# Kernel tuning notes

Hardware: AMD Instinct MI355X
Metric: run time of the kernel (lower is better)

Reference implementation:

```python
import jax, jax.numpy as jnp
import numpy as np

NET_W = 416.0
NET_H = 416.0
OBJ_THRESH = 0.5
COORD_SCALE = 5.0
NOOBJ_SCALE = 1.0
OBJ_SCALE = 5.0
CLASS_SCALE = 1.0


def setup_inputs() -> dict:
    key = jax.random.key(0)
    k1, k2, k3, k4, k5, k6, k7 = jax.random.split(key, 7)
    B, A, C, gh, gw = 32, 5, 80, 52, 52
    HW = gh * gw
    net_out = jax.random.normal(k1, (B, gh, gw, A * (5 + C)), dtype=jnp.float32)
    anchors = jnp.array([[10., 13.], [33., 23.], [62., 45.], [116., 90.], [373., 326.]], dtype=jnp.float32)
    obj_cell = (jax.random.uniform(k2, (B, HW)) < 0.01).astype(jnp.float32)  # [B,HW]
    a_idx = jax.random.randint(k3, (B, HW), 0, A)
    a_onehot = jax.nn.one_hot(a_idx, A, axis=1, dtype=jnp.float32)  # [B,A,HW]
    anchor_mask = (obj_cell[:, None, :] * a_onehot)[:, :, None, :]  # [B,A,1,HW]
    obj_mask = (obj_cell[:, None, :] * jnp.ones((1, A, 1), jnp.float32))  # [B,A,HW]
    # targets: [x_off, y_off, w_log, h_log, conf, class] per anchor/cell, zero where unassigned
    t_xy = jax.random.uniform(k4, (B, A, 2, HW), dtype=jnp.float32)
    t_wh = 0.5 * jax.random.normal(k5, (B, A, 2, HW), dtype=jnp.float32)
    t_conf = jax.random.uniform(k6, (B, A, 1, HW), dtype=jnp.float32)
    t_cls = jax.random.randint(k7, (B, A, 1, HW), 0, C).astype(jnp.float32)
    targets = jnp.concatenate([t_xy, t_wh, t_conf, t_cls], axis=2) * anchor_mask
    return {"net_out": net_out, "targets": targets, "anchor_mask": anchor_mask,
            "obj_mask": obj_mask, "anchors": anchors}


def _to_grid(coords, col, row, gw, gh, aw, ah):
    # coords: [B,A,4,HW] (xy offsets in-cell, wh in log space) -> corner boxes [B,A,4,HW]
    cx = (coords[:, :, 0, :] + col) / gw * NET_W
    cy = (coords[:, :, 1, :] + row) / gh * NET_H
    w = jnp.exp(coords[:, :, 2, :]) * aw
    h = jnp.exp(coords[:, :, 3, :]) * ah
    x1 = cx - 0.5 * w
    y1 = cy - 0.5 * h
    return jnp.stack([x1, y1, x1 + w, y1 + h], axis=2)


def _yolo_loss(net_out, targets, anchor_mask, obj_mask, anchors):
    B, gh, gw, oc = net_out.shape
    A = anchors.shape[0]
    C = oc // A - 5
    HW = gh * gw
    p = net_out.reshape(B, A, 5 + C, HW)
    xy = jax.nn.sigmoid(p[:, :, :2, :])            # [B,A,2,HW]
    wh = p[:, :, 2:4, :]                           # raw log-space
    conf = jax.nn.sigmoid(p[:, :, 4, :])           # [B,A,HW]
    logits = p[:, :, 5:, :]                        # [B,A,C,HW]
    conf_mask = anchor_mask[:, :, 0, :]            # [B,A,HW]

    # class cross-entropy, masked to responsible anchors
    logp = jax.nn.log_softmax(logits, axis=2)
    t_cls = targets[:, :, 5, :].astype(jnp.int32)  # [B,A,HW]
    ce = -jnp.take_along_axis(logp, t_cls[:, :, None, :], axis=2)[:, :, 0, :]
    clas_loss = (ce * conf_mask).sum()

    aw = anchors[:, 0][None, :, None]
    ah = anchors[:, 1][None, :, None]
    true_xy = targets[:, :, 0:2, :]
    true_wh = targets[:, :, 2:4, :]
    t_wscale = jnp.exp(true_wh[:, :, 0, :]) * aw / NET_W
    t_hscale = jnp.exp(true_wh[:, :, 1, :]) * ah / NET_H
    p_wscale = jnp.exp(wh[:, :, 0, :]) * aw / NET_W
    p_hscale = jnp.exp(wh[:, :, 1, :]) * ah / NET_H
    xy_loss = (jnp.square(xy - true_xy) * anchor_mask).sum()
    wh_loss = (jnp.square(p_wscale - t_wscale) * conf_mask).sum() \
            + (jnp.square(p_hscale - t_hscale) * conf_mask).sum()
    coords_loss = xy_loss + wh_loss

    t_conf = targets[:, :, 4, :]
    diff2 = jnp.square(conf - t_conf)
    obj_conf_loss = (diff2 * conf_mask).sum()
    noobj1 = diff2 * (1.0 - obj_mask)
    no_resp = (1.0 - conf_mask) * obj_mask

    hw = jnp.arange(HW)
    col = (hw % gw).astype(jnp.float32)
    row = (hw // gw).astype(jnp.float32)
    pred_boxes = _to_grid(jnp.concatenate([xy, wh], axis=2), col, row, gw, gh, aw, ah)
    gt_boxes = _to_grid(targets[:, :, :4, :], col, row, gw, gh, aw, ah)
    iw = jnp.maximum(jnp.minimum(pred_boxes[:, :, 2, :], gt_boxes[:, :, 2, :])
                     - jnp.maximum(pred_boxes[:, :, 0, :], gt_boxes[:, :, 0, :]), 0.0)
    ih = jnp.maximum(jnp.minimum(pred_boxes[:, :, 3, :], gt_boxes[:, :, 3, :])
                     - jnp.maximum(pred_boxes[:, :, 1, :], gt_boxes[:, :, 1, :]), 0.0)
    inter = iw * ih
    area_p = (pred_boxes[:, :, 2, :] - pred_boxes[:, :, 0, :]) * (pred_boxes[:, :, 3, :] - pred_boxes[:, :, 1, :])
    area_g = (gt_boxes[:, :, 2, :] - gt_boxes[:, :, 0, :]) * (gt_boxes[:, :, 3, :] - gt_boxes[:, :, 1, :])
    iou = inter / (area_p + area_g - inter + 1e-9)
    iou_lt = (iou < OBJ_THRESH).astype(jnp.float32)
    noobj_conf_loss = (noobj1 + diff2 * no_resp * iou_lt).sum()

    total = (clas_loss * CLASS_SCALE + coords_loss * COORD_SCALE
             + obj_conf_loss * OBJ_SCALE + noobj_conf_loss * NOOBJ_SCALE)
    return total


def reference(net_out, targets, anchor_mask, obj_mask, anchors):
    return _yolo_loss(net_out, targets, anchor_mask, obj_mask, anchors)
```

## Files before the change

### kernel.cpp

```cpp
#include <hip/hip_runtime.h>


constexpr int B_  = 32;
constexpr int A_  = 5;
constexpr int C_  = 80;
constexpr int GW_ = 52;
constexpr int GH_ = 52;
constexpr int HW_ = GW_ * GH_;
constexpr int NCH = 5 + C_;
constexpr int TOTAL = B_ * A_ * HW_;
constexpr int BLOCK = 256;
constexpr int GRID  = TOTAL / BLOCK;

constexpr float NET_W = 416.0f;
constexpr float NET_H = 416.0f;
constexpr float OBJ_THRESH  = 0.5f;
constexpr float COORD_SCALE = 5.0f;
constexpr float NOOBJ_SCALE = 1.0f;
constexpr float OBJ_SCALE   = 5.0f;
constexpr float CLASS_SCALE = 1.0f;

__device__ __forceinline__ float sigmoidf_(float x) {
    return 1.0f / (1.0f + __expf(-x));
}

__global__ __launch_bounds__(256) void yolo_partial_kernel(
    const float* __restrict__ net,
    const float* __restrict__ tgt,
    const float* __restrict__ amask,
    const float* __restrict__ omask,
    const float* __restrict__ anchors,
    float* __restrict__ partial)
{
    const int i    = blockIdx.x * blockDim.x + threadIdx.x;
    const int lane = threadIdx.x & 63;

    const int hw = i % HW_;
    const int ba = i / HW_;
    const int a  = ba % A_;

    const unsigned nbase = (unsigned)ba * (unsigned)(NCH * HW_) + (unsigned)hw;
    const unsigned tbase = (unsigned)ba * (unsigned)(6 * HW_)   + (unsigned)hw;

    const float cm = amask[i];
    const float om = omask[i];

    const bool want_ce  = (cm != 0.0f);
    const bool need_box = want_ce || (om != 0.0f);

    const float conf = sigmoidf_(net[nbase + 4u * HW_]);
    float t_conf = 0.0f;
    if (want_ce) t_conf = tgt[tbase + 4u * HW_];
    const float d     = conf - t_conf;
    const float diff2 = d * d;

    float loss = diff2 * (1.0f - om) * NOOBJ_SCALE;

    int tc = 0;
    if (need_box) {
        const float aw = anchors[2 * a];
        const float ah = anchors[2 * a + 1];

        const float p0 = net[nbase + 0u * HW_];
        const float p1 = net[nbase + 1u * HW_];
        const float p2 = net[nbase + 2u * HW_];
        const float p3 = net[nbase + 3u * HW_];
        const float t0 = tgt[tbase + 0u * HW_];
        const float t1 = tgt[tbase + 1u * HW_];
        const float t2 = tgt[tbase + 2u * HW_];
        const float t3 = tgt[tbase + 3u * HW_];

        const float sx = sigmoidf_(p0);
        const float sy = sigmoidf_(p1);

        if (want_ce) {
            const float dx = sx - t0;
            const float dy = sy - t1;
            const float pws = __expf(p2) * aw * (1.0f / NET_W);
            const float phs = __expf(p3) * ah * (1.0f / NET_H);
            const float tws = __expf(t2) * aw * (1.0f / NET_W);
            const float ths = __expf(t3) * ah * (1.0f / NET_H);
            const float dw = pws - tws;
            const float dh = phs - ths;
            loss += (dx * dx + dy * dy + dw * dw + dh * dh) * COORD_SCALE;
            loss += diff2 * OBJ_SCALE;
            tc = (int)tgt[tbase + 5u * HW_];
        } else {
            const float col = (float)(hw % GW_);
            const float row = (float)(hw / GW_);

            const float pcx = (sx + col) * (NET_W / (float)GW_);
            const float pcy = (sy + row) * (NET_H / (float)GH_);
            const float pw  = __expf(p2) * aw;
            const float ph  = __expf(p3) * ah;
            const float px1 = pcx - 0.5f * pw;
            const float py1 = pcy - 0.5f * ph;
            const float px2 = px1 + pw;
            const float py2 = py1 + ph;

            const float gcx = (t0 + col) * (NET_W / (float)GW_);
            const float gcy = (t1 + row) * (NET_H / (float)GH_);
            const float gwd = __expf(t2) * aw;
            const float ghd = __expf(t3) * ah;
            const float gx1 = gcx - 0.5f * gwd;
            const float gy1 = gcy - 0.5f * ghd;
            const float gx2 = gx1 + gwd;
            const float gy2 = gy1 + ghd;

            const float iw = fmaxf(fminf(px2, gx2) - fmaxf(px1, gx1), 0.0f);
            const float ih = fmaxf(fminf(py2, gy2) - fmaxf(py1, gy1), 0.0f);
            const float inter  = iw * ih;
            const float area_p = (px2 - px1) * (py2 - py1);
            const float area_g = (gx2 - gx1) * (gy2 - gy1);
            const float iou = inter / (area_p + area_g - inter + 1e-9f);
            if (iou < OBJ_THRESH) {
                loss += diff2 * NOOBJ_SCALE;
            }
        }
    }

    unsigned long long m = __ballot(want_ce);
    while (m) {
        const int src = __ffsll((long long)m) - 1;
        m &= m - 1;
        const unsigned nb  = (unsigned)__shfl((int)nbase, src, 64);
        const int      tcs = __shfl(tc, src, 64);

        const float x0 = net[nb + (unsigned)(5 + lane) * HW_];
        const float x1 = (lane < 16) ? net[nb + (unsigned)(69 + lane) * HW_]
                                     : -1e30f;

        float mx = fmaxf(x0, x1);
        #pragma unroll
        for (int off = 32; off > 0; off >>= 1)
            mx = fmaxf(mx, __shfl_xor(mx, off, 64));

        float s = __expf(x0 - mx) + ((lane < 16) ? __expf(x1 - mx) : 0.0f);
        #pragma unroll
        for (int off = 32; off > 0; off >>= 1)
            s += __shfl_xor(s, off, 64);

        const int  idx = (tcs < 64) ? tcs : (tcs - 64);
        const float xa = __shfl(x0, idx, 64);
        const float xb = __shfl(x1, idx, 64);
        const float xt = (tcs < 64) ? xa : xb;

        const float ce = -(xt - mx - __logf(s));
        if (lane == src) loss += ce * CLASS_SCALE;
    }

    #pragma unroll
    for (int off = 32; off > 0; off >>= 1)
        loss += __shfl_down(loss, off, 64);

    __shared__ float wsum[4];
    const int wid = threadIdx.x >> 6;
    if (lane == 0) wsum[wid] = loss;
    __syncthreads();
    if (threadIdx.x == 0)
        partial[blockIdx.x] = wsum[0] + wsum[1] + wsum[2] + wsum[3];
}

__global__ __launch_bounds__(256) void yolo_reduce_kernel(
    const float* __restrict__ partial, float* __restrict__ out)
{
    float s = 0.0f;
    for (int j = threadIdx.x; j < GRID; j += BLOCK)
        s += partial[j];

    #pragma unroll
    for (int off = 32; off > 0; off >>= 1)
        s += __shfl_down(s, off, 64);

    __shared__ float w[4];
    const int lane = threadIdx.x & 63;
    const int wid  = threadIdx.x >> 6;
    if (lane == 0) w[wid] = s;
    __syncthreads();
    if (threadIdx.x == 0)
        out[0] = w[0] + w[1] + w[2] + w[3];
}

extern "C" void kernel_launch(void* const* d_in, const int* in_sizes, int n_in,
                              void* d_out, int out_size, void* d_ws, size_t ws_size,
                              hipStream_t stream) {
    const float* net     = (const float*)d_in[0];
    const float* tgt     = (const float*)d_in[1];
    const float* amask   = (const float*)d_in[2];
    const float* omask   = (const float*)d_in[3];
    const float* anchors = (const float*)d_in[4];
    float* out     = (float*)d_out;
    float* partial = (float*)d_ws;

    yolo_partial_kernel<<<GRID, BLOCK, 0, stream>>>(net, tgt, amask, omask, anchors, partial);
    yolo_reduce_kernel<<<1, BLOCK, 0, stream>>>(partial, out);
}
```

Before: 11.94 us.

## Process two cells per thread, pair softmax rows, fuse reduction via atomics

```diff
diff --git a/kernel.cpp b/kernel.cpp
--- a/kernel.cpp
+++ b/kernel.cpp
@@ -10,7 +10,8 @@
 constexpr int NCH = 5 + C_;
 constexpr int TOTAL = B_ * A_ * HW_;
 constexpr int BLOCK = 256;
-constexpr int GRID  = TOTAL / BLOCK;
+constexpr int CPT   = 2;
+constexpr int GRID  = TOTAL / (BLOCK * CPT);
 
 constexpr float NET_W = 416.0f;
 constexpr float NET_H = 416.0f;
@@ -24,129 +25,185 @@
     return 1.0f / (1.0f + __expf(-x));
 }
 
-__global__ __launch_bounds__(256) void yolo_partial_kernel(
+__device__ __forceinline__ float cell_terms(
+    const float* __restrict__ net, const float* __restrict__ tgt,
+    unsigned nbase, unsigned tbase, int hw, float aw, float ah,
+    float cm, float om, float diff2, bool want_ce, int& tc)
+{
+    float loss = diff2 * (1.0f - om) * NOOBJ_SCALE;
+
+    const bool need_box = want_ce || (om != 0.0f);
+    if (!need_box) return loss;
+
+    const float p0 = net[nbase + 0u * HW_];
+    const float p1 = net[nbase + 1u * HW_];
+    const float p2 = net[nbase + 2u * HW_];
+    const float p3 = net[nbase + 3u * HW_];
+    const float t0 = tgt[tbase + 0u * HW_];
+    const float t1 = tgt[tbase + 1u * HW_];
+    const float t2 = tgt[tbase + 2u * HW_];
+    const float t3 = tgt[tbase + 3u * HW_];
+
+    const float sx = sigmoidf_(p0);
+    const float sy = sigmoidf_(p1);
+
+    if (want_ce) {
+        const float dx = sx - t0;
+        const float dy = sy - t1;
+        const float pws = __expf(p2) * aw * (1.0f / NET_W);
+        const float phs = __expf(p3) * ah * (1.0f / NET_H);
+        const float tws = __expf(t2) * aw * (1.0f / NET_W);
+        const float ths = __expf(t3) * ah * (1.0f / NET_H);
+        const float dw = pws - tws;
+        const float dh = phs - ths;
+        loss += (dx * dx + dy * dy + dw * dw + dh * dh) * COORD_SCALE;
+        loss += diff2 * OBJ_SCALE;
+        tc = (int)tgt[tbase + 5u * HW_];
+    } else {
+        const float col = (float)(hw % GW_);
+        const float row = (float)(hw / GW_);
+
+        const float pcx = (sx + col) * (NET_W / (float)GW_);
+        const float pcy = (sy + row) * (NET_H / (float)GH_);
+        const float pw  = __expf(p2) * aw;
+        const float ph  = __expf(p3) * ah;
+        const float px1 = pcx - 0.5f * pw;
+        const float py1 = pcy - 0.5f * ph;
+        const float px2 = px1 + pw;
+        const float py2 = py1 + ph;
+
+        const float gcx = (t0 + col) * (NET_W / (float)GW_);
+        const float gcy = (t1 + row) * (NET_H / (float)GH_);
+        const float gwd = __expf(t2) * aw;
+        const float ghd = __expf(t3) * ah;
+        const float gx1 = gcx - 0.5f * gwd;
+        const float gy1 = gcy - 0.5f * ghd;
+        const float gx2 = gx1 + gwd;
+        const float gy2 = gy1 + ghd;
+
+        const float iw = fmaxf(fminf(px2, gx2) - fmaxf(px1, gx1), 0.0f);
+        const float ih = fmaxf(fminf(py2, gy2) - fmaxf(py1, gy1), 0.0f);
+        const float inter  = iw * ih;
+        const float area_p = (px2 - px1) * (py2 - py1);
+        const float area_g = (gx2 - gx1) * (gy2 - gy1);
+        const float iou = inter / (area_p + area_g - inter + 1e-9f);
+        if (iou < OBJ_THRESH) loss += diff2 * NOOBJ_SCALE;
+    }
+    return loss;
+}
+
+__global__ __launch_bounds__(256) void yolo_loss_kernel(
     const float* __restrict__ net,
     const float* __restrict__ tgt,
     const float* __restrict__ amask,
     const float* __restrict__ omask,
     const float* __restrict__ anchors,
-    float* __restrict__ partial)
+    float* __restrict__ out)
 {
-    const int i    = blockIdx.x * blockDim.x + threadIdx.x;
+    const int t    = blockIdx.x * blockDim.x + threadIdx.x;
     const int lane = threadIdx.x & 63;
 
-    const int hw = i % HW_;
-    const int ba = i / HW_;
-    const int a  = ba % A_;
-
-    const unsigned nbase = (unsigned)ba * (unsigned)(NCH * HW_) + (unsigned)hw;
-    const unsigned tbase = (unsigned)ba * (unsigned)(6 * HW_)   + (unsigned)hw;
-
-    const float cm = amask[i];
-    const float om = omask[i];
-
-    const bool want_ce  = (cm != 0.0f);
-    const bool need_box = want_ce || (om != 0.0f);
-
-    const float conf = sigmoidf_(net[nbase + 4u * HW_]);
-    float t_conf = 0.0f;
-    if (want_ce) t_conf = tgt[tbase + 4u * HW_];
-    const float d     = conf - t_conf;
-    const float diff2 = d * d;
-
-    float loss = diff2 * (1.0f - om) * NOOBJ_SCALE;
-
-    int tc = 0;
-    if (need_box) {
-        const float aw = anchors[2 * a];
-        const float ah = anchors[2 * a + 1];
-
-        const float p0 = net[nbase + 0u * HW_];
-        const float p1 = net[nbase + 1u * HW_];
-        const float p2 = net[nbase + 2u * HW_];
-        const float p3 = net[nbase + 3u * HW_];
-        const float t0 = tgt[tbase + 0u * HW_];
-        const float t1 = tgt[tbase + 1u * HW_];
-        const float t2 = tgt[tbase + 2u * HW_];
-        const float t3 = tgt[tbase + 3u * HW_];
-
-        const float sx = sigmoidf_(p0);
-        const float sy = sigmoidf_(p1);
-
-        if (want_ce) {
-            const float dx = sx - t0;
-            const float dy = sy - t1;
-            const float pws = __expf(p2) * aw * (1.0f / NET_W);
-            const float phs = __expf(p3) * ah * (1.0f / NET_H);
-            const float tws = __expf(t2) * aw * (1.0f / NET_W);
-            const float ths = __expf(t3) * ah * (1.0f / NET_H);
-            const float dw = pws - tws;
-            const float dh = phs - ths;
-            loss += (dx * dx + dy * dy + dw * dw + dh * dh) * COORD_SCALE;
-            loss += diff2 * OBJ_SCALE;
-            tc = (int)tgt[tbase + 5u * HW_];
-        } else {
-            const float col = (float)(hw % GW_);
-            const float row = (float)(hw / GW_);
-
-            const float pcx = (sx + col) * (NET_W / (float)GW_);
-            const float pcy = (sy + row) * (NET_H / (float)GH_);
-            const float pw  = __expf(p2) * aw;
-            const float ph  = __expf(p3) * ah;
-            const float px1 = pcx - 0.5f * pw;
-            const float py1 = pcy - 0.5f * ph;
-            const float px2 = px1 + pw;
-            const float py2 = py1 + ph;
-
-            const float gcx = (t0 + col) * (NET_W / (float)GW_);
-            const float gcy = (t1 + row) * (NET_H / (float)GH_);
-            const float gwd = __expf(t2) * aw;
-            const float ghd = __expf(t3) * ah;
-            const float gx1 = gcx - 0.5f * gwd;
-            const float gy1 = gcy - 0.5f * ghd;
-            const float gx2 = gx1 + gwd;
-            const float gy2 = gy1 + ghd;
-
-            const float iw = fmaxf(fminf(px2, gx2) - fmaxf(px1, gx1), 0.0f);
-            const float ih = fmaxf(fminf(py2, gy2) - fmaxf(py1, gy1), 0.0f);
-            const float inter  = iw * ih;
-            const float area_p = (px2 - px1) * (py2 - py1);
-            const float area_g = (gx2 - gx1) * (gy2 - gy1);
-            const float iou = inter / (area_p + area_g - inter + 1e-9f);
-            if (iou < OBJ_THRESH) {
-                loss += diff2 * NOOBJ_SCALE;
+    const int cell0 = 2 * t;
+    const int hw0   = cell0 % HW_;
+    const int ba    = cell0 / HW_;
+    const int a     = ba % A_;
+
+    const unsigned nbase0 = (unsigned)ba * (unsigned)(NCH * HW_) + (unsigned)hw0;
+    const unsigned tbase0 = (unsigned)ba * (unsigned)(6 * HW_)   + (unsigned)hw0;
+
+    const float2 am2 = *reinterpret_cast<const float2*>(amask + cell0);
+    const float2 om2 = *reinterpret_cast<const float2*>(omask + cell0);
+    const float2 cf2 = *reinterpret_cast<const float2*>(net + nbase0 + 4u * HW_);
+
+    const float aw = anchors[2 * a];
+    const float ah = anchors[2 * a + 1];
+
+    float loss = 0.0f;
+    int   tc0 = 0, tc1 = 0;
+
+    const bool ce0 = (am2.x != 0.0f);
+    {
+        const float conf  = sigmoidf_(cf2.x);
+        const float tcf   = ce0 ? tgt[tbase0 + 4u * HW_] : 0.0f;
+        const float d     = conf - tcf;
+        const float diff2 = d * d;
+        loss += cell_terms(net, tgt, nbase0, tbase0, hw0, aw, ah,
+                           am2.x, om2.x, diff2, ce0, tc0);
+        if (ce0) loss += 0.0f;
+    }
+    const bool ce1 = (am2.y != 0.0f);
+    {
+        const float conf  = sigmoidf_(cf2.y);
+        const float tcf   = ce1 ? tgt[tbase0 + 1u + 4u * HW_] : 0.0f;
+        const float d     = conf - tcf;
+        const float diff2 = d * d;
+        loss += cell_terms(net, tgt, nbase0 + 1u, tbase0 + 1u, hw0 + 1, aw, ah,
+                           am2.y, om2.y, diff2, ce1, tc1);
+    }
+
+    {
+        unsigned long long m0 = __ballot(ce0);
+        unsigned long long m1 = __ballot(ce1);
+        const int nb0i = (int)nbase0;
+        while (m0 | m1) {
+            int srcA, slotA;
+            if (m0) { srcA = __ffsll((long long)m0) - 1; slotA = 0; m0 &= m0 - 1; }
+            else    { srcA = __ffsll((long long)m1) - 1; slotA = 1; m1 &= m1 - 1; }
+            const bool hasB = (m0 | m1) != 0ull;
+            int srcB = 0, slotB = 0;
+            if (hasB) {
+                if (m0) { srcB = __ffsll((long long)m0) - 1; slotB = 0; m0 &= m0 - 1; }
+                else    { srcB = __ffsll((long long)m1) - 1; slotB = 1; m1 &= m1 - 1; }
+            }
+
+            const unsigned nbA = (unsigned)__shfl(nb0i, srcA, 64) + (unsigned)slotA;
+            const int      tcA = slotA ? __shfl(tc1, srcA, 64) : __shfl(tc0, srcA, 64);
+
+            const float xA0 = net[nbA + (unsigned)(5 + lane) * HW_];
+            const float xA1 = (lane < 16) ? net[nbA + (unsigned)(69 + lane) * HW_] : -1e30f;
+
+            float xB0 = 0.0f, xB1 = -1e30f;
+            unsigned nbB = 0; int tcB = 0;
+            if (hasB) {
+                nbB = (unsigned)__shfl(nb0i, srcB, 64) + (unsigned)slotB;
+                tcB = slotB ? __shfl(tc1, srcB, 64) : __shfl(tc0, srcB, 64);
+                xB0 = net[nbB + (unsigned)(5 + lane) * HW_];
+                xB1 = (lane < 16) ? net[nbB + (unsigned)(69 + lane) * HW_] : -1e30f;
+            }
+
+            {
+                float mx = fmaxf(xA0, xA1);
+                #pragma unroll
+                for (int off = 32; off > 0; off >>= 1)
+                    mx = fmaxf(mx, __shfl_xor(mx, off, 64));
+                float s = __expf(xA0 - mx) + ((lane < 16) ? __expf(xA1 - mx) : 0.0f);
+                #pragma unroll
+                for (int off = 32; off > 0; off >>= 1)
+                    s += __shfl_xor(s, off, 64);
+                const int idx = (tcA < 64) ? tcA : (tcA - 64);
+                const float xa = __shfl(xA0, idx, 64);
+                const float xb = __shfl(xA1, idx, 64);
+                const float xt = (tcA < 64) ? xa : xb;
+                const float ce = -(xt - mx - __logf(s));
+                if (lane == srcA) loss += ce * CLASS_SCALE;
+            }
+            if (hasB) {
+                float mx = fmaxf(xB0, xB1);
+                #pragma unroll
+                for (int off = 32; off > 0; off >>= 1)
+                    mx = fmaxf(mx, __shfl_xor(mx, off, 64));
+                float s = __expf(xB0 - mx) + ((lane < 16) ? __expf(xB1 - mx) : 0.0f);
+                #pragma unroll
+                for (int off = 32; off > 0; off >>= 1)
+                    s += __shfl_xor(s, off, 64);
+                const int idx = (tcB < 64) ? tcB : (tcB - 64);
+                const float xa = __shfl(xB0, idx, 64);
+                const float xb = __shfl(xB1, idx, 64);
+                const float xt = (tcB < 64) ? xa : xb;
+                const float ce = -(xt - mx - __logf(s));
+                if (lane == srcB) loss += ce * CLASS_SCALE;
             }
         }
-    }
-
-    unsigned long long m = __ballot(want_ce);
-    while (m) {
-        const int src = __ffsll((long long)m) - 1;
-        m &= m - 1;
-        const unsigned nb  = (unsigned)__shfl((int)nbase, src, 64);
-        const int      tcs = __shfl(tc, src, 64);
-
-        const float x0 = net[nb + (unsigned)(5 + lane) * HW_];
-        const float x1 = (lane < 16) ? net[nb + (unsigned)(69 + lane) * HW_]
-                                     : -1e30f;
-
-        float mx = fmaxf(x0, x1);
-        #pragma unroll
-        for (int off = 32; off > 0; off >>= 1)
-            mx = fmaxf(mx, __shfl_xor(mx, off, 64));
-
-        float s = __expf(x0 - mx) + ((lane < 16) ? __expf(x1 - mx) : 0.0f);
-        #pragma unroll
-        for (int off = 32; off > 0; off >>= 1)
-            s += __shfl_xor(s, off, 64);
-
-        const int  idx = (tcs < 64) ? tcs : (tcs - 64);
-        const float xa = __shfl(x0, idx, 64);
-        const float xb = __shfl(x1, idx, 64);
-        const float xt = (tcs < 64) ? xa : xb;
-
-        const float ce = -(xt - mx - __logf(s));
-        if (lane == src) loss += ce * CLASS_SCALE;
     }
 
     #pragma unroll
@@ -158,27 +215,7 @@
     if (lane == 0) wsum[wid] = loss;
     __syncthreads();
     if (threadIdx.x == 0)
-        partial[blockIdx.x] = wsum[0] + wsum[1] + wsum[2] + wsum[3];
-}
-
-__global__ __launch_bounds__(256) void yolo_reduce_kernel(
-    const float* __restrict__ partial, float* __restrict__ out)
-{
-    float s = 0.0f;
-    for (int j = threadIdx.x; j < GRID; j += BLOCK)
-        s += partial[j];
-
-    #pragma unroll
-    for (int off = 32; off > 0; off >>= 1)
-        s += __shfl_down(s, off, 64);
-
-    __shared__ float w[4];
-    const int lane = threadIdx.x & 63;
-    const int wid  = threadIdx.x >> 6;
-    if (lane == 0) w[wid] = s;
-    __syncthreads();
-    if (threadIdx.x == 0)
-        out[0] = w[0] + w[1] + w[2] + w[3];
+        atomicAdd(out, wsum[0] + wsum[1] + wsum[2] + wsum[3]);
 }
 
 extern "C" void kernel_launch(void* const* d_in, const int* in_sizes, int n_in,
@@ -189,9 +226,9 @@
     const float* amask   = (const float*)d_in[2];
     const float* omask   = (const float*)d_in[3];
     const float* anchors = (const float*)d_in[4];
-    float* out     = (float*)d_out;
-    float* partial = (float*)d_ws;
-
-    yolo_partial_kernel<<<GRID, BLOCK, 0, stream>>>(net, tgt, amask, omask, anchors, partial);
-    yolo_reduce_kernel<<<1, BLOCK, 0, stream>>>(partial, out);
-}
+    float* out = (float*)d_out;
+
+    hipMemsetAsync(out, 0, sizeof(float), stream);
+
+    yolo_loss_kernel<<<GRID, BLOCK, 0, stream>>>(net, tgt, amask, omask, anchors, out);
+}
```

After: 23.18 us. 1.94x slower.

## Fuse final reduction via last-block counter and batch four CE rows per wave

Applied to the files above, without the earlier changes.

```diff
diff --git a/kernel.cpp b/kernel.cpp
--- a/kernel.cpp
+++ b/kernel.cpp
@@ -24,13 +24,15 @@
     return 1.0f / (1.0f + __expf(-x));
 }
 
-__global__ __launch_bounds__(256) void yolo_partial_kernel(
+__global__ __launch_bounds__(256) void yolo_loss_kernel(
     const float* __restrict__ net,
     const float* __restrict__ tgt,
     const float* __restrict__ amask,
     const float* __restrict__ omask,
     const float* __restrict__ anchors,
-    float* __restrict__ partial)
+    float* __restrict__ partial,
+    unsigned* __restrict__ counter,
+    float* __restrict__ out)
 {
     const int i    = blockIdx.x * blockDim.x + threadIdx.x;
     const int lane = threadIdx.x & 63;
@@ -113,40 +115,63 @@
             const float area_p = (px2 - px1) * (py2 - py1);
             const float area_g = (gx2 - gx1) * (gy2 - gy1);
             const float iou = inter / (area_p + area_g - inter + 1e-9f);
-            if (iou < OBJ_THRESH) {
-                loss += diff2 * NOOBJ_SCALE;
-            }
+            if (iou < OBJ_THRESH) loss += diff2 * NOOBJ_SCALE;
         }
     }
 
-    unsigned long long m = __ballot(want_ce);
-    while (m) {
-        const int src = __ffsll((long long)m) - 1;
-        m &= m - 1;
-        const unsigned nb  = (unsigned)__shfl((int)nbase, src, 64);
-        const int      tcs = __shfl(tc, src, 64);
-
-        const float x0 = net[nb + (unsigned)(5 + lane) * HW_];
-        const float x1 = (lane < 16) ? net[nb + (unsigned)(69 + lane) * HW_]
-                                     : -1e30f;
-
-        float mx = fmaxf(x0, x1);
-        #pragma unroll
-        for (int off = 32; off > 0; off >>= 1)
-            mx = fmaxf(mx, __shfl_xor(mx, off, 64));
-
-        float s = __expf(x0 - mx) + ((lane < 16) ? __expf(x1 - mx) : 0.0f);
-        #pragma unroll
-        for (int off = 32; off > 0; off >>= 1)
-            s += __shfl_xor(s, off, 64);
-
-        const int  idx = (tcs < 64) ? tcs : (tcs - 64);
-        const float xa = __shfl(x0, idx, 64);
-        const float xb = __shfl(x1, idx, 64);
-        const float xt = (tcs < 64) ? xa : xb;
-
-        const float ce = -(xt - mx - __logf(s));
-        if (lane == src) loss += ce * CLASS_SCALE;
+    {
+        unsigned long long m = __ballot(want_ce);
+        const int nb_i = (int)nbase;
+        const int g    = lane >> 4;
+        const int j    = lane & 15;
+        while (m) {
+            int s0 = __ffsll((long long)m) - 1; m &= m - 1;
+            int cnt = 1, s1 = s0, s2 = s0, s3 = s0;
+            if (m) { s1 = __ffsll((long long)m) - 1; m &= m - 1; cnt = 2;
+                if (m) { s2 = __ffsll((long long)m) - 1; m &= m - 1; cnt = 3;
+                    if (m) { s3 = __ffsll((long long)m) - 1; m &= m - 1; cnt = 4; } } }
+
+            const int src_mine = (g == 0) ? s0 : (g == 1) ? s1 : (g == 2) ? s2 : s3;
+            const unsigned nb  = (unsigned)__shfl(nb_i, src_mine, 64);
+            const int      tce = __shfl(tc, src_mine, 64);
+
+            const float x0 = net[nb + (unsigned)(5 + j +  0) * HW_];
+            const float x1 = net[nb + (unsigned)(5 + j + 16) * HW_];
+            const float x2 = net[nb + (unsigned)(5 + j + 32) * HW_];
+            const float x3 = net[nb + (unsigned)(5 + j + 48) * HW_];
+            const float x4 = net[nb + (unsigned)(5 + j + 64) * HW_];
+
+            float mx = fmaxf(fmaxf(fmaxf(x0, x1), fmaxf(x2, x3)), x4);
+            #pragma unroll
+            for (int off = 8; off > 0; off >>= 1)
+                mx = fmaxf(mx, __shfl_xor(mx, off, 64));
+
+            float sm = __expf(x0 - mx) + __expf(x1 - mx) + __expf(x2 - mx)
+                     + __expf(x3 - mx) + __expf(x4 - mx);
+            #pragma unroll
+            for (int off = 8; off > 0; off >>= 1)
+                sm += __shfl_xor(sm, off, 64);
+
+            const int j0 = tce & 15;
+            const int k0 = tce >> 4;
+            const float xk = (k0 == 0) ? x0 : (k0 == 1) ? x1 : (k0 == 2) ? x2
+                           : (k0 == 3) ? x3 : x4;
+            float cand = (j == j0) ? xk : -1e30f;
+            #pragma unroll
+            for (int off = 8; off > 0; off >>= 1)
+                cand = fmaxf(cand, __shfl_xor(cand, off, 64));
+
+            const float ce = -(cand - mx - __logf(sm));
+
+            const float ce0 = __shfl(ce,  0, 64);
+            const float ce1 = __shfl(ce, 16, 64);
+            const float ce2 = __shfl(ce, 32, 64);
+            const float ce3 = __shfl(ce, 48, 64);
+            if (lane == s0)             loss += ce0 * CLASS_SCALE;
+            if (cnt > 1 && lane == s1)  loss += ce1 * CLASS_SCALE;
+            if (cnt > 2 && lane == s2)  loss += ce2 * CLASS_SCALE;
+            if (cnt > 3 && lane == s3)  loss += ce3 * CLASS_SCALE;
+        }
     }
 
     #pragma unroll
@@ -154,31 +179,36 @@
         loss += __shfl_down(loss, off, 64);
 
     __shared__ float wsum[4];
+    __shared__ int   isLast;
     const int wid = threadIdx.x >> 6;
     if (lane == 0) wsum[wid] = loss;
     __syncthreads();
-    if (threadIdx.x == 0)
+
+    if (threadIdx.x == 0) {
         partial[blockIdx.x] = wsum[0] + wsum[1] + wsum[2] + wsum[3];
-}
-
-__global__ __launch_bounds__(256) void yolo_reduce_kernel(
-    const float* __restrict__ partial, float* __restrict__ out)
-{
-    float s = 0.0f;
-    for (int j = threadIdx.x; j < GRID; j += BLOCK)
-        s += partial[j];
-
-    #pragma unroll
-    for (int off = 32; off > 0; off >>= 1)
-        s += __shfl_down(s, off, 64);
-
-    __shared__ float w[4];
-    const int lane = threadIdx.x & 63;
-    const int wid  = threadIdx.x >> 6;
-    if (lane == 0) w[wid] = s;
+        __threadfence();
+        const unsigned t = atomicAdd(counter, 1u);
+        const int last = ((t % (unsigned)GRID) == (unsigned)(GRID - 1));
+        isLast = last;
+        if (last) atomicSub(counter, (unsigned)GRID);
+    }
     __syncthreads();
-    if (threadIdx.x == 0)
-        out[0] = w[0] + w[1] + w[2] + w[3];
+
+    if (isLast) {
+        __threadfence();
+        float s = 0.0f;
+        for (int p = threadIdx.x; p < GRID; p += BLOCK)
+            s += __hip_atomic_load(&partial[p], __ATOMIC_RELAXED,
+                                   __HIP_MEMORY_SCOPE_AGENT);
+        #pragma unroll
+        for (int off = 32; off > 0; off >>= 1)
+            s += __shfl_down(s, off, 64);
+        __shared__ float w2[4];
+        if (lane == 0) w2[wid] = s;
+        __syncthreads();
+        if (threadIdx.x == 0)
+            out[0] = w2[0] + w2[1] + w2[2] + w2[3];
+    }
 }
 
 extern "C" void kernel_launch(void* const* d_in, const int* in_sizes, int n_in,
@@ -189,9 +219,10 @@
     const float* amask   = (const float*)d_in[2];
     const float* omask   = (const float*)d_in[3];
     const float* anchors = (const float*)d_in[4];
-    float* out     = (float*)d_out;
-    float* partial = (float*)d_ws;
-
-    yolo_partial_kernel<<<GRID, BLOCK, 0, stream>>>(net, tgt, amask, omask, anchors, partial);
-    yolo_reduce_kernel<<<1, BLOCK, 0, stream>>>(partial, out);
+    float*    out     = (float*)d_out;
+    float*    partial = (float*)d_ws;
+    unsigned* counter = (unsigned*)d_ws + GRID;
+
+    yolo_loss_kernel<<<GRID, BLOCK, 0, stream>>>(net, tgt, amask, omask, anchors,
+                                                 partial, counter, out);
 }
```

Result: slower. 39.13 us (+227.8%).

## Process four cells per thread with vector loads and batch four CE events per wave

Applied to the files above, without the earlier changes.

```diff
diff --git a/kernel.cpp b/kernel.cpp
--- a/kernel.cpp
+++ b/kernel.cpp
@@ -10,7 +10,8 @@
 constexpr int NCH = 5 + C_;
 constexpr int TOTAL = B_ * A_ * HW_;
 constexpr int BLOCK = 256;
-constexpr int GRID  = TOTAL / BLOCK;
+constexpr int CPT   = 4;
+constexpr int GRID  = (TOTAL + BLOCK * CPT - 1) / (BLOCK * CPT);
 
 constexpr float NET_W = 416.0f;
 constexpr float NET_H = 416.0f;
@@ -22,6 +23,73 @@
 
 __device__ __forceinline__ float sigmoidf_(float x) {
     return 1.0f / (1.0f + __expf(-x));
+}
+
+__device__ __forceinline__ float cell_terms(
+    const float* __restrict__ net, const float* __restrict__ tgt,
+    unsigned nbase, unsigned tbase, int hw, float aw, float ah,
+    float om, float diff2, bool want_ce, int& tc)
+{
+    float loss = diff2 * (1.0f - om) * NOOBJ_SCALE;
+
+    const bool need_box = want_ce || (om != 0.0f);
+    if (!need_box) return loss;
+
+    const float p0 = net[nbase + 0u * HW_];
+    const float p1 = net[nbase + 1u * HW_];
+    const float p2 = net[nbase + 2u * HW_];
+    const float p3 = net[nbase + 3u * HW_];
+    const float t0 = tgt[tbase + 0u * HW_];
+    const float t1 = tgt[tbase + 1u * HW_];
+    const float t2 = tgt[tbase + 2u * HW_];
+    const float t3 = tgt[tbase + 3u * HW_];
+
+    const float sx = sigmoidf_(p0);
+    const float sy = sigmoidf_(p1);
+
+    if (want_ce) {
+        const float dx = sx - t0;
+        const float dy = sy - t1;
+        const float pws = __expf(p2) * aw * (1.0f / NET_W);
+        const float phs = __expf(p3) * ah * (1.0f / NET_H);
+        const float tws = __expf(t2) * aw * (1.0f / NET_W);
+        const float ths = __expf(t3) * ah * (1.0f / NET_H);
+        const float dw = pws - tws;
+        const float dh = phs - ths;
+        loss += (dx * dx + dy * dy + dw * dw + dh * dh) * COORD_SCALE;
+        loss += diff2 * OBJ_SCALE;
+        tc = (int)tgt[tbase + 5u * HW_];
+    } else {
+        const float col = (float)(hw % GW_);
+        const float row = (float)(hw / GW_);
+
+        const float pcx = (sx + col) * (NET_W / (float)GW_);
+        const float pcy = (sy + row) * (NET_H / (float)GH_);
+        const float pw  = __expf(p2) * aw;
+        const float ph  = __expf(p3) * ah;
+        const float px1 = pcx - 0.5f * pw;
+        const float py1 = pcy - 0.5f * ph;
+        const float px2 = px1 + pw;
+        const float py2 = py1 + ph;
+
+        const float gcx = (t0 + col) * (NET_W / (float)GW_);
+        const float gcy = (t1 + row) * (NET_H / (float)GH_);
+        const float gwd = __expf(t2) * aw;
+        const float ghd = __expf(t3) * ah;
+        const float gx1 = gcx - 0.5f * gwd;
+        const float gy1 = gcy - 0.5f * ghd;
+        const float gx2 = gx1 + gwd;
+        const float gy2 = gy1 + ghd;
+
+        const float iw = fmaxf(fminf(px2, gx2) - fmaxf(px1, gx1), 0.0f);
+        const float ih = fmaxf(fminf(py2, gy2) - fmaxf(py1, gy1), 0.0f);
+        const float inter  = iw * ih;
+        const float area_p = (px2 - px1) * (py2 - py1);
+        const float area_g = (gx2 - gx1) * (gy2 - gy1);
+        const float iou = inter / (area_p + area_g - inter + 1e-9f);
+        if (iou < OBJ_THRESH) loss += diff2 * NOOBJ_SCALE;
+    }
+    return loss;
 }
 
 __global__ __launch_bounds__(256) void yolo_partial_kernel(
@@ -32,121 +100,134 @@
     const float* __restrict__ anchors,
     float* __restrict__ partial)
 {
-    const int i    = blockIdx.x * blockDim.x + threadIdx.x;
+    const int t    = blockIdx.x * blockDim.x + threadIdx.x;
     const int lane = threadIdx.x & 63;
 
-    const int hw = i % HW_;
-    const int ba = i / HW_;
-    const int a  = ba % A_;
-
-    const unsigned nbase = (unsigned)ba * (unsigned)(NCH * HW_) + (unsigned)hw;
-    const unsigned tbase = (unsigned)ba * (unsigned)(6 * HW_)   + (unsigned)hw;
-
-    const float cm = amask[i];
-    const float om = omask[i];
-
-    const bool want_ce  = (cm != 0.0f);
-    const bool need_box = want_ce || (om != 0.0f);
-
-    const float conf = sigmoidf_(net[nbase + 4u * HW_]);
-    float t_conf = 0.0f;
-    if (want_ce) t_conf = tgt[tbase + 4u * HW_];
-    const float d     = conf - t_conf;
-    const float diff2 = d * d;
-
-    float loss = diff2 * (1.0f - om) * NOOBJ_SCALE;
-
-    int tc = 0;
-    if (need_box) {
+    const int  cell0 = CPT * t;
+    const bool act   = (cell0 < TOTAL);
+
+    float loss = 0.0f;
+    bool ces0 = false, ces1 = false, ces2 = false, ces3 = false;
+    int  tc0 = 0, tc1 = 0, tc2 = 0, tc3 = 0;
+    unsigned nbase0 = 0;
+
+    if (act) {
+        const int hw0 = cell0 % HW_;
+        const int ba  = cell0 / HW_;
+        const int a   = ba % A_;
+
+        nbase0 = (unsigned)ba * (unsigned)(NCH * HW_) + (unsigned)hw0;
+        const unsigned tbase0 = (unsigned)ba * (unsigned)(6 * HW_) + (unsigned)hw0;
+
+        const float4 am4 = *reinterpret_cast<const float4*>(amask + cell0);
+        const float4 om4 = *reinterpret_cast<const float4*>(omask + cell0);
+        const float4 cf4 = *reinterpret_cast<const float4*>(net + nbase0 + 4u * HW_);
+
         const float aw = anchors[2 * a];
         const float ah = anchors[2 * a + 1];
 
-        const float p0 = net[nbase + 0u * HW_];
-        const float p1 = net[nbase + 1u * HW_];
-        const float p2 = net[nbase + 2u * HW_];
-        const float p3 = net[nbase + 3u * HW_];
-        const float t0 = tgt[tbase + 0u * HW_];
-        const float t1 = tgt[tbase + 1u * HW_];
-        const float t2 = tgt[tbase + 2u * HW_];
-        const float t3 = tgt[tbase + 3u * HW_];
-
-        const float sx = sigmoidf_(p0);
-        const float sy = sigmoidf_(p1);
-
-        if (want_ce) {
-            const float dx = sx - t0;
-            const float dy = sy - t1;
-            const float pws = __expf(p2) * aw * (1.0f / NET_W);
-            const float phs = __expf(p3) * ah * (1.0f / NET_H);
-            const float tws = __expf(t2) * aw * (1.0f / NET_W);
-            const float ths = __expf(t3) * ah * (1.0f / NET_H);
-            const float dw = pws - tws;
-            const float dh = phs - ths;
-            loss += (dx * dx + dy * dy + dw * dw + dh * dh) * COORD_SCALE;
-            loss += diff2 * OBJ_SCALE;
-            tc = (int)tgt[tbase + 5u * HW_];
-        } else {
-            const float col = (float)(hw % GW_);
-            const float row = (float)(hw / GW_);
-
-            const float pcx = (sx + col) * (NET_W / (float)GW_);
-            const float pcy = (sy + row) * (NET_H / (float)GH_);
-            const float pw  = __expf(p2) * aw;
-            const float ph  = __expf(p3) * ah;
-            const float px1 = pcx - 0.5f * pw;
-            const float py1 = pcy - 0.5f * ph;
-            const float px2 = px1 + pw;
-            const float py2 = py1 + ph;
-
-            const float gcx = (t0 + col) * (NET_W / (float)GW_);
-            const float gcy = (t1 + row) * (NET_H / (float)GH_);
-            const float gwd = __expf(t2) * aw;
-            const float ghd = __expf(t3) * ah;
-            const float gx1 = gcx - 0.5f * gwd;
-            const float gy1 = gcy - 0.5f * ghd;
-            const float gx2 = gx1 + gwd;
-            const float gy2 = gy1 + ghd;
-
-            const float iw = fmaxf(fminf(px2, gx2) - fmaxf(px1, gx1), 0.0f);
-            const float ih = fmaxf(fminf(py2, gy2) - fmaxf(py1, gy1), 0.0f);
-            const float inter  = iw * ih;
-            const float area_p = (px2 - px1) * (py2 - py1);
-            const float area_g = (gx2 - gx1) * (gy2 - gy1);
-            const float iou = inter / (area_p + area_g - inter + 1e-9f);
-            if (iou < OBJ_THRESH) {
-                loss += diff2 * NOOBJ_SCALE;
-            }
+        {
+            ces0 = (am4.x != 0.0f);
+            const float conf  = sigmoidf_(cf4.x);
+            const float tcf   = ces0 ? tgt[tbase0 + 0u + 4u * HW_] : 0.0f;
+            const float d     = conf - tcf;
+            loss += cell_terms(net, tgt, nbase0 + 0u, tbase0 + 0u, hw0 + 0,
+                               aw, ah, om4.x, d * d, ces0, tc0);
+        }
+        {
+            ces1 = (am4.y != 0.0f);
+            const float conf  = sigmoidf_(cf4.y);
+            const float tcf   = ces1 ? tgt[tbase0 + 1u + 4u * HW_] : 0.0f;
+            const float d     = conf - tcf;
+            loss += cell_terms(net, tgt, nbase0 + 1u, tbase0 + 1u, hw0 + 1,
+                               aw, ah, om4.y, d * d, ces1, tc1);
+        }
+        {
+            ces2 = (am4.z != 0.0f);
+            const float conf  = sigmoidf_(cf4.z);
+            const float tcf   = ces2 ? tgt[tbase0 + 2u + 4u * HW_] : 0.0f;
+            const float d     = conf - tcf;
+            loss += cell_terms(net, tgt, nbase0 + 2u, tbase0 + 2u, hw0 + 2,
+                               aw, ah, om4.z, d * d, ces2, tc2);
+        }
+        {
+            ces3 = (am4.w != 0.0f);
+            const float conf  = sigmoidf_(cf4.w);
+            const float tcf   = ces3 ? tgt[tbase0 + 3u + 4u * HW_] : 0.0f;
+            const float d     = conf - tcf;
+            loss += cell_terms(net, tgt, nbase0 + 3u, tbase0 + 3u, hw0 + 3,
+                               aw, ah, om4.w, d * d, ces3, tc3);
         }
     }
 
-    unsigned long long m = __ballot(want_ce);
-    while (m) {
-        const int src = __ffsll((long long)m) - 1;
-        m &= m - 1;
-        const unsigned nb  = (unsigned)__shfl((int)nbase, src, 64);
-        const int      tcs = __shfl(tc, src, 64);
-
-        const float x0 = net[nb + (unsigned)(5 + lane) * HW_];
-        const float x1 = (lane < 16) ? net[nb + (unsigned)(69 + lane) * HW_]
-                                     : -1e30f;
-
-        float mx = fmaxf(x0, x1);
-        #pragma unroll
-        for (int off = 32; off > 0; off >>= 1)
-            mx = fmaxf(mx, __shfl_xor(mx, off, 64));
-
-        float s = __expf(x0 - mx) + ((lane < 16) ? __expf(x1 - mx) : 0.0f);
-        #pragma unroll
-        for (int off = 32; off > 0; off >>= 1)
-            s += __shfl_xor(s, off, 64);
-
-        const int  idx = (tcs < 64) ? tcs : (tcs - 64);
-        const float xa = __shfl(x0, idx, 64);
-        const float xb = __shfl(x1, idx, 64);
-        const float xt = (tcs < 64) ? xa : xb;
-
-        const float ce = -(xt - mx - __logf(s));
-        if (lane == src) loss += ce * CLASS_SCALE;
+    {
+        unsigned long long m0 = __ballot(ces0);
+        unsigned long long m1 = __ballot(ces1);
+        unsigned long long m2 = __ballot(ces2);
+        unsigned long long m3 = __ballot(ces3);
+
+        const int nb_i = (int)nbase0;
+        const int tcpack = (tc0 & 0xff) | ((tc1 & 0xff) << 8)
+                         | ((tc2 & 0xff) << 16) | ((tc3 & 0xff) << 24);
+        const int g = lane >> 4;
+        const int j = lane & 15;
+
+        while (m0 | m1 | m2 | m3) {
+            int e0 = -1, e1 = -1, e2 = -1, e3 = -1;
+#define POP_EV(dst)                                                          \
+            if (m0)      { dst = (__ffsll((long long)m0) - 1);            m0 &= m0 - 1; } \
+            else if (m1) { dst = (__ffsll((long long)m1) - 1) | (1 << 6); m1 &= m1 - 1; } \
+            else if (m2) { dst = (__ffsll((long long)m2) - 1) | (2 << 6); m2 &= m2 - 1; } \
+            else if (m3) { dst = (__ffsll((long long)m3) - 1) | (3 << 6); m3 &= m3 - 1; }
+            POP_EV(e0); POP_EV(e1); POP_EV(e2); POP_EV(e3);
+#undef POP_EV
+
+            const int evg  = (g == 0) ? e0 : (g == 1) ? e1 : (g == 2) ? e2 : e3;
+            const int ev   = (evg >= 0) ? evg : e0;
+            const int src  = ev & 63;
+            const int slot = ev >> 6;
+
+            const unsigned nb = (unsigned)__shfl(nb_i, src, 64) + (unsigned)slot;
+            const int tp  = __shfl(tcpack, src, 64);
+            const int tce = (tp >> (8 * slot)) & 0xff;
+
+            const float x0 = net[nb + (unsigned)(5 + j +  0) * HW_];
+            const float x1 = net[nb + (unsigned)(5 + j + 16) * HW_];
+            const float x2 = net[nb + (unsigned)(5 + j + 32) * HW_];
+            const float x3 = net[nb + (unsigned)(5 + j + 48) * HW_];
+            const float x4 = net[nb + (unsigned)(5 + j + 64) * HW_];
+
+            float mx = fmaxf(fmaxf(fmaxf(x0, x1), fmaxf(x2, x3)), x4);
+            #pragma unroll
+            for (int off = 8; off > 0; off >>= 1)
+                mx = fmaxf(mx, __shfl_xor(mx, off, 64));
+
+            float sm = __expf(x0 - mx) + __expf(x1 - mx) + __expf(x2 - mx)
+                     + __expf(x3 - mx) + __expf(x4 - mx);
+            #pragma unroll
+            for (int off = 8; off > 0; off >>= 1)
+                sm += __shfl_xor(sm, off, 64);
+
+            const int j0 = tce & 15;
+            const int k0 = tce >> 4;
+            const float xk = (k0 == 0) ? x0 : (k0 == 1) ? x1 : (k0 == 2) ? x2
+                           : (k0 == 3) ? x3 : x4;
+            float cand = (j == j0) ? xk : -1e30f;
+            #pragma unroll
+            for (int off = 8; off > 0; off >>= 1)
+                cand = fmaxf(cand, __shfl_xor(cand, off, 64));
+
+            const float ce = -(cand - mx - __logf(sm));
+
+            const float c0 = __shfl(ce,  0, 64);
+            const float c1 = __shfl(ce, 16, 64);
+            const float c2 = __shfl(ce, 32, 64);
+            const float c3 = __shfl(ce, 48, 64);
+            if (e0 >= 0 && lane == (e0 & 63)) loss += c0 * CLASS_SCALE;
+            if (e1 >= 0 && lane == (e1 & 63)) loss += c1 * CLASS_SCALE;
+            if (e2 >= 0 && lane == (e2 & 63)) loss += c2 * CLASS_SCALE;
+            if (e3 >= 0 && lane == (e3 & 63)) loss += c3 * CLASS_SCALE;
+        }
     }
 
     #pragma unroll
@@ -165,8 +246,8 @@
     const float* __restrict__ partial, float* __restrict__ out)
 {
     float s = 0.0f;
-    for (int j = threadIdx.x; j < GRID; j += BLOCK)
-        s += partial[j];
+    for (int p = threadIdx.x; p < GRID; p += BLOCK)
+        s += partial[p];
 
     #pragma unroll
     for (int off = 32; off > 0; off >>= 1)
```

After: 12.67 us. 1.06x slower.
